# Kernel tuning notes

Measured on AMD Instinct MI355X. Metric: run time of the kernel, lower is better.

Reference implementation:

```python
import jax, jax.numpy as jnp
import numpy as np

IN_CH = 16
OUT_CH = 64
G = 4
K = 3
EXP_CH = G * IN_CH * OUT_CH  # 4096 expanded channels
SET_LEN = G * IN_CH          # 64 indices per pooling set
B, H, W = 8, 56, 56


def setup_inputs() -> dict:
    key = jax.random.key(0)
    k1, k2, k3, k4 = jax.random.split(key, 4)
    x = jax.random.normal(k1, (B, IN_CH, H, W), dtype=jnp.float32)
    # grouped conv weight: [out_channels=EXP_CH, in_ch/groups=1, K, K]
    weight = jax.random.normal(k2, (EXP_CH, 1, K, K), dtype=jnp.float32) * 0.1
    bias = jax.random.normal(k3, (EXP_CH,), dtype=jnp.float32) * 0.1
    # channel_idx_sets: OUT_CH sets, each SET_LEN indices into the EXP_CH channels
    idx_sets = jax.random.randint(k4, (OUT_CH, SET_LEN), 0, EXP_CH, dtype=jnp.int32)
    return {"x": x, "weight": weight, "bias": bias, "idx_sets": idx_sets}


def reference(x, weight, bias, idx_sets):
    # Grouped conv2d: groups = IN_CH, output channels = G*IN_CH*OUT_CH
    out = jax.lax.conv_general_dilated(
        x, weight,
        window_strides=(1, 1),
        padding=((1, 1), (1, 1)),
        feature_group_count=IN_CH,
        dimension_numbers=("NCHW", "OIHW", "NCHW"),
    )
    out = out + bias[None, :, None, None]  # [B, EXP_CH, H, W]
    # FusedMultiPool: for each output channel j, max over channels idx_sets[j]
    gathered = out[:, idx_sets]            # [B, OUT_CH, SET_LEN, H, W]
    return jnp.max(gathered, axis=2)       # [B, OUT_CH, H, W]
```

## Files before the change

### kernel.cpp

```cpp
#include <hip/hip_runtime.h>

#define IN_CH    16
#define OUT_CH   64
#define SET_LEN  64
#define BB       8
#define HH       56
#define WW       56

#define TILEROWS 8
#define NTILES   7
#define LDSROWS  (TILEROWS + 2)
#define LROW     56
#define LDS_XN   (IN_CH * LDSROWS * LROW)
#define NVEC     (IN_CH * LDSROWS * 14)

#define WS_NEEDED (OUT_CH * SET_LEN * 12 * 4)

typedef float f32x2 __attribute__((ext_vector_type(2)));
typedef float f32x4 __attribute__((ext_vector_type(4)));

static __device__ __forceinline__ f32x2 splat2(float s) { return (f32x2){s, s}; }

static __device__ __forceinline__ f32x2 pk_mul_slo(unsigned long long sp, f32x2 b) {
    f32x2 d;
    asm("v_pk_mul_f32 %0, %1, %2 op_sel:[0,0] op_sel_hi:[0,1]"
        : "=v"(d) : "s"(sp), "v"(b));
    return d;
}
static __device__ __forceinline__ f32x2 pk_mul_shi(unsigned long long sp, f32x2 b) {
    f32x2 d;
    asm("v_pk_mul_f32 %0, %1, %2 op_sel:[1,0] op_sel_hi:[1,1]"
        : "=v"(d) : "s"(sp), "v"(b));
    return d;
}
static __device__ __forceinline__ f32x2 pk_fma_slo(unsigned long long sp, f32x2 b, f32x2 c) {
    f32x2 d;
    asm("v_pk_fma_f32 %0, %1, %2, %3 op_sel:[0,0,0] op_sel_hi:[0,1,1]"
        : "=v"(d) : "s"(sp), "v"(b), "v"(c));
    return d;
}
static __device__ __forceinline__ f32x2 pk_fma_shi(unsigned long long sp, f32x2 b, f32x2 c) {
    f32x2 d;
    asm("v_pk_fma_f32 %0, %1, %2, %3 op_sel:[1,0,0] op_sel_hi:[1,1,1]"
        : "=v"(d) : "s"(sp), "v"(b), "v"(c));
    return d;
}
static __device__ __forceinline__ f32x2 pk_add_vv(f32x2 a, f32x2 b) {
    f32x2 d;
    asm("v_pk_add_f32 %0, %1, %2 op_sel:[0,0] op_sel_hi:[1,1]"
        : "=v"(d) : "v"(a), "v"(b));
    return d;
}
static __device__ __forceinline__ f32x2 pk_add_shi(unsigned long long sp, f32x2 b) {
    f32x2 d;
    asm("v_pk_add_f32 %0, %1, %2 op_sel:[1,0] op_sel_hi:[1,1]"
        : "=v"(d) : "s"(sp), "v"(b));
    return d;
}

__global__ __launch_bounds__(64)
void rptn_presort(const float* __restrict__ w, const float* __restrict__ bias,
                  const int* __restrict__ idx, float* __restrict__ ws_w) {
    const int oc = blockIdx.x;
    const int t  = threadIdx.x;
    __shared__ int cnt[IN_CH], pos[IN_CH], eord[SET_LEN];

    if (t < IN_CH) cnt[t] = 0;
    __syncthreads();
    const int e = idx[oc * SET_LEN + t];
    const int c = e >> 8;
    atomicAdd(&cnt[c], 1);
    __syncthreads();
    if (t == 0) {
        int run = 0;
        for (int i = 0; i < IN_CH; ++i) { pos[i] = run; run += cnt[i]; }
    }
    __syncthreads();
    const int p = atomicAdd(&pos[c], 1);
    eord[p] = e;
    __syncthreads();

    const int    es  = eord[t];
    float*       dst = ws_w + ((size_t)oc * SET_LEN + t) * 12;
    const float* src = w + es * 9;
    #pragma unroll
    for (int i = 0; i < 9; ++i) dst[i] = src[i];
    dst[9]  = bias[es];
    dst[10] = __int_as_float(es >> 8);
    dst[11] = 0.0f;
}

__global__ __launch_bounds__(256, 2)
void rptn_fused_kernel(const float* __restrict__ x,
                       const float* __restrict__ ws_w,
                       float*       __restrict__ out) {
    const int oc   = blockIdx.x;
    const int tile = blockIdx.y;
    const int b    = blockIdx.z;
    const int tid  = threadIdx.x;
    const int tx   = tid & 63;
    const int grp  = __builtin_amdgcn_readfirstlane(tid >> 6);

    __shared__ float s_x[LDS_XN];

    const int r0 = tile * TILEROWS;
    const float* xb = x + (size_t)b * IN_CH * HH * WW;
    #pragma unroll
    for (int it = 0; it < 9; ++it) {
        const int v = tid + it * 256;
        if (it < 8 || v < NVEC) {
            const int c   = v / (LDSROWS * 14);
            const int rem = v - c * (LDSROWS * 14);
            const int r   = rem / 14;
            const int q   = rem - r * 14;
            const int gr  = r0 - 1 + r;
            f32x4 val = {0, 0, 0, 0};
            if ((unsigned)gr < (unsigned)HH)
                val = *(const f32x4*)(xb + (c * HH + gr) * WW + q * 4);
            *(f32x4*)&s_x[(c * LDSROWS + r) * LROW + q * 4] = val;
        }
    }
    __syncthreads();

    const bool  lanev = (tx < WW);
    const int   txr   = lanev ? tx : 0;
    const int   txl   = (txr > 0)  ? txr - 1 : 0;
    const int   txp   = (txr < 55) ? txr + 1 : 55;
    const float lm    = (txr == 0)  ? 0.0f : 1.0f;
    const float rm    = (txr == 55) ? 0.0f : 1.0f;

    f32x2 acc = { -__builtin_inff(), -__builtin_inff() };
    int ccur = -1;
    f32x2 v00={0,0},v01={0,0},v02={0,0};
    f32x2 v10={0,0},v11={0,0},v12={0,0};
    f32x2 v20={0,0},v21={0,0},v22={0,0};

    const ulonglong2* wt = (const ulonglong2*)ws_w + (size_t)oc * SET_LEN * 3;

    #pragma unroll 4
    for (int k = 0; k < SET_LEN; ++k) {
        const ulonglong2 A = wt[k * 3 + 0];
        const ulonglong2 B = wt[k * 3 + 1];
        const ulonglong2 C = wt[k * 3 + 2];
        const int c = (int)(unsigned int)(C.y & 0xffffffffULL);
        if (c != ccur) {
            ccur = c;
            const float* sp = &s_x[(c * LDSROWS + grp * 2) * LROW];
            const float n00=sp[txl]*lm,        n01=sp[txr],        n02=sp[txp]*rm;
            const float n10=sp[LROW+txl]*lm,   n11=sp[LROW+txr],   n12=sp[LROW+txp]*rm;
            const float n20=sp[2*LROW+txl]*lm, n21=sp[2*LROW+txr], n22=sp[2*LROW+txp]*rm;
            const float n30=sp[3*LROW+txl]*lm, n31=sp[3*LROW+txr], n32=sp[3*LROW+txp]*rm;
            v00=(f32x2){n00,n10}; v01=(f32x2){n01,n11}; v02=(f32x2){n02,n12};
            v10=(f32x2){n10,n20}; v11=(f32x2){n11,n21}; v12=(f32x2){n12,n22};
            v20=(f32x2){n20,n30}; v21=(f32x2){n21,n31}; v22=(f32x2){n22,n32};
        }
        f32x2 t0 = pk_mul_slo(A.x, v00);
        t0       = pk_fma_shi(A.x, v01, t0);
        t0       = pk_fma_slo(A.y, v02, t0);
        f32x2 t1 = pk_mul_shi(A.y, v10);
        t1       = pk_fma_slo(B.x, v11, t1);
        t1       = pk_fma_shi(B.x, v12, t1);
        f32x2 t2 = pk_mul_slo(B.y, v20);
        t2       = pk_fma_shi(B.y, v21, t2);
        t2       = pk_fma_slo(C.x, v22, t2);
        f32x2 s  = pk_add_vv(t0, t1);
        s        = pk_add_vv(s, t2);
        s        = pk_add_shi(C.x, s);
        acc.x = fmaxf(acc.x, s.x);
        acc.y = fmaxf(acc.y, s.y);
    }

    if (lanev) {
        const size_t o = (((size_t)b * OUT_CH + oc) * HH + (r0 + grp * 2)) * WW + tx;
        out[o]      = acc.x;
        out[o + WW] = acc.y;
    }
}

__global__ __launch_bounds__(256, 2)
void rptn_fused_fallback(const float* __restrict__ x,
                         const float* __restrict__ w,
                         const float* __restrict__ bias,
                         const int*   __restrict__ idx,
                         float*       __restrict__ out) {
    const int oc   = blockIdx.x;
    const int tile = blockIdx.y;
    const int b    = blockIdx.z;
    const int tid  = threadIdx.x;
    const int tx   = tid & 63;
    const int grp  = __builtin_amdgcn_readfirstlane(tid >> 6);

    __shared__ float s_x[LDS_XN];
    __shared__ f32x4 s_w[SET_LEN * 3];
    __shared__ int   s_cnt[IN_CH];
    __shared__ int   s_pos[IN_CH];
    __shared__ int   s_eord[SET_LEN];

    if (tid < IN_CH) s_cnt[tid] = 0;
    __syncthreads();
    int my_e = 0;
    if (tid < SET_LEN) {
        my_e = idx[oc * SET_LEN + tid];
        atomicAdd(&s_cnt[my_e >> 8], 1);
    }
    __syncthreads();
    if (tid == 0) {
        int run = 0;
        for (int c = 0; c < IN_CH; ++c) { s_pos[c] = run; run += s_cnt[c]; }
    }
    __syncthreads();
    if (tid < SET_LEN) {
        int p = atomicAdd(&s_pos[my_e >> 8], 1);
        s_eord[p] = my_e;
    }
    __syncthreads();

    float* s_wf = (float*)s_w;
    for (int i = tid; i < SET_LEN * 12; i += 256) {
        const int j    = i / 12;
        const int comp = i - j * 12;
        const int e    = s_eord[j];
        float v;
        if (comp < 9)        v = w[e * 9 + comp];
        else if (comp == 9)  v = bias[e];
        else if (comp == 10) v = __int_as_float(e >> 8);
        else                 v = 0.0f;
        s_wf[j * 12 + comp] = v;
    }

    const int r0 = tile * TILEROWS;
    const float* xb = x + (size_t)b * IN_CH * HH * WW;
    #pragma unroll
    for (int it = 0; it < 9; ++it) {
        const int v = tid + it * 256;
        if (it < 8 || v < NVEC) {
            const int c   = v / (LDSROWS * 14);
            const int rem = v - c * (LDSROWS * 14);
            const int r   = rem / 14;
            const int q   = rem - r * 14;
            const int gr  = r0 - 1 + r;
            f32x4 val = {0, 0, 0, 0};
            if ((unsigned)gr < (unsigned)HH)
                val = *(const f32x4*)(xb + (c * HH + gr) * WW + q * 4);
            *(f32x4*)&s_x[(c * LDSROWS + r) * LROW + q * 4] = val;
        }
    }
    __syncthreads();

    const bool  lanev = (tx < WW);
    const int   txr   = lanev ? tx : 0;
    const int   txl   = (txr > 0)  ? txr - 1 : 0;
    const int   txp   = (txr < 55) ? txr + 1 : 55;
    const float lm    = (txr == 0)  ? 0.0f : 1.0f;
    const float rm    = (txr == 55) ? 0.0f : 1.0f;

    f32x2 acc = { -__builtin_inff(), -__builtin_inff() };
    int ccur = -1;
    f32x2 v00={0,0},v01={0,0},v02={0,0};
    f32x2 v10={0,0},v11={0,0},v12={0,0};
    f32x2 v20={0,0},v21={0,0},v22={0,0};

    #pragma unroll 2
    for (int k = 0; k < SET_LEN; ++k) {
        const f32x4 q0 = s_w[k * 3 + 0];
        const f32x4 q1 = s_w[k * 3 + 1];
        const f32x4 q2 = s_w[k * 3 + 2];
        const int c = __float_as_int(q2.z);
        if (c != ccur) {
            ccur = c;
            const float* sp = &s_x[(c * LDSROWS + grp * 2) * LROW];
            const float n00=sp[txl]*lm,        n01=sp[txr],        n02=sp[txp]*rm;
            const float n10=sp[LROW+txl]*lm,   n11=sp[LROW+txr],   n12=sp[LROW+txp]*rm;
            const float n20=sp[2*LROW+txl]*lm, n21=sp[2*LROW+txr], n22=sp[2*LROW+txp]*rm;
            const float n30=sp[3*LROW+txl]*lm, n31=sp[3*LROW+txr], n32=sp[3*LROW+txp]*rm;
            v00=(f32x2){n00,n10}; v01=(f32x2){n01,n11}; v02=(f32x2){n02,n12};
            v10=(f32x2){n10,n20}; v11=(f32x2){n11,n21}; v12=(f32x2){n12,n22};
            v20=(f32x2){n20,n30}; v21=(f32x2){n21,n31}; v22=(f32x2){n22,n32};
        }
        f32x2 t0 = __builtin_elementwise_fma(splat2(q0.z), v02,
                   __builtin_elementwise_fma(splat2(q0.y), v01,
                   __builtin_elementwise_fma(splat2(q0.x), v00, splat2(q2.y))));
        f32x2 t1 = __builtin_elementwise_fma(splat2(q1.y), v12,
                   __builtin_elementwise_fma(splat2(q1.x), v11,
                                             splat2(q0.w) * v10));
        f32x2 t2 = __builtin_elementwise_fma(splat2(q2.x), v22,
                   __builtin_elementwise_fma(splat2(q1.w), v21,
                                             splat2(q1.z) * v20));
        const f32x2 s = t0 + (t1 + t2);
        acc.x = fmaxf(acc.x, s.x);
        acc.y = fmaxf(acc.y, s.y);
    }

    if (lanev) {
        const size_t o = (((size_t)b * OUT_CH + oc) * HH + (r0 + grp * 2)) * WW + tx;
        out[o]      = acc.x;
        out[o + WW] = acc.y;
    }
}

extern "C" void kernel_launch(void* const* d_in, const int* in_sizes, int n_in,
                              void* d_out, int out_size, void* d_ws, size_t ws_size,
                              hipStream_t stream) {
    const float* x    = (const float*)d_in[0];
    const float* w    = (const float*)d_in[1];
    const float* bias = (const float*)d_in[2];
    const int*   idx  = (const int*)d_in[3];
    float*       out  = (float*)d_out;

    dim3 grid(OUT_CH, NTILES, BB);
    dim3 block(256);

    if (ws_size >= (size_t)WS_NEEDED) {
        float* ws_w = (float*)d_ws;
        rptn_presort<<<dim3(OUT_CH), dim3(64), 0, stream>>>(w, bias, idx, ws_w);
        rptn_fused_kernel<<<grid, block, 0, stream>>>(x, ws_w, out);
    } else {
        rptn_fused_fallback<<<grid, block, 0, stream>>>(x, w, bias, idx, out);
    }
}
```

Baseline: 116.8 us.

## Pack channel ids into scalar words and fully unroll pooling loop with vector weight loads

The presort kernel now also writes eight packed 32-bit words per output channel holding the 4-bit input-channel id of each sorted entry, so the main kernel can decide neighbourhood reloads from wave-uniform scalar bits. The 64-entry loop is fully unrolled, and the weights are read through a VGPR-offset base (a forced v_mov zero) so they arrive as vector loads fed to the packed math as VGPR operands. The goal is to remove per-iteration scalar load latency and loop overhead. In exchange it adds a larger code body, extra VGPR pressure, and per-lane redundant weight loads.

New measurement: 166.4 us. +42.5%, slower.

```diff
diff --git a/kernel.cpp b/kernel.cpp
--- a/kernel.cpp
+++ b/kernel.cpp
@@ -14,35 +14,37 @@
 #define LDS_XN   (IN_CH * LDSROWS * LROW)
 #define NVEC     (IN_CH * LDSROWS * 14)
 
-#define WS_NEEDED (OUT_CH * SET_LEN * 12 * 4)
+#define WS_CW_OFF 0
+#define WS_W_OFF  2048
+#define WS_NEEDED (WS_W_OFF + OUT_CH * SET_LEN * 12 * 4)
 
 typedef float f32x2 __attribute__((ext_vector_type(2)));
 typedef float f32x4 __attribute__((ext_vector_type(4)));
 
 static __device__ __forceinline__ f32x2 splat2(float s) { return (f32x2){s, s}; }
 
-static __device__ __forceinline__ f32x2 pk_mul_slo(unsigned long long sp, f32x2 b) {
+static __device__ __forceinline__ f32x2 pk_mul_vlo(unsigned long long wp, f32x2 b) {
     f32x2 d;
     asm("v_pk_mul_f32 %0, %1, %2 op_sel:[0,0] op_sel_hi:[0,1]"
-        : "=v"(d) : "s"(sp), "v"(b));
-    return d;
-}
-static __device__ __forceinline__ f32x2 pk_mul_shi(unsigned long long sp, f32x2 b) {
+        : "=v"(d) : "v"(wp), "v"(b));
+    return d;
+}
+static __device__ __forceinline__ f32x2 pk_mul_vhi(unsigned long long wp, f32x2 b) {
     f32x2 d;
     asm("v_pk_mul_f32 %0, %1, %2 op_sel:[1,0] op_sel_hi:[1,1]"
-        : "=v"(d) : "s"(sp), "v"(b));
-    return d;
-}
-static __device__ __forceinline__ f32x2 pk_fma_slo(unsigned long long sp, f32x2 b, f32x2 c) {
+        : "=v"(d) : "v"(wp), "v"(b));
+    return d;
+}
+static __device__ __forceinline__ f32x2 pk_fma_vlo(unsigned long long wp, f32x2 b, f32x2 c) {
     f32x2 d;
     asm("v_pk_fma_f32 %0, %1, %2, %3 op_sel:[0,0,0] op_sel_hi:[0,1,1]"
-        : "=v"(d) : "s"(sp), "v"(b), "v"(c));
-    return d;
-}
-static __device__ __forceinline__ f32x2 pk_fma_shi(unsigned long long sp, f32x2 b, f32x2 c) {
+        : "=v"(d) : "v"(wp), "v"(b), "v"(c));
+    return d;
+}
+static __device__ __forceinline__ f32x2 pk_fma_vhi(unsigned long long wp, f32x2 b, f32x2 c) {
     f32x2 d;
     asm("v_pk_fma_f32 %0, %1, %2, %3 op_sel:[1,0,0] op_sel_hi:[1,1,1]"
-        : "=v"(d) : "s"(sp), "v"(b), "v"(c));
+        : "=v"(d) : "v"(wp), "v"(b), "v"(c));
     return d;
 }
 static __device__ __forceinline__ f32x2 pk_add_vv(f32x2 a, f32x2 b) {
@@ -51,16 +53,17 @@
         : "=v"(d) : "v"(a), "v"(b));
     return d;
 }
-static __device__ __forceinline__ f32x2 pk_add_shi(unsigned long long sp, f32x2 b) {
+static __device__ __forceinline__ f32x2 pk_add_vhi(unsigned long long wp, f32x2 b) {
     f32x2 d;
     asm("v_pk_add_f32 %0, %1, %2 op_sel:[1,0] op_sel_hi:[1,1]"
-        : "=v"(d) : "s"(sp), "v"(b));
+        : "=v"(d) : "v"(wp), "v"(b));
     return d;
 }
 
 __global__ __launch_bounds__(64)
 void rptn_presort(const float* __restrict__ w, const float* __restrict__ bias,
-                  const int* __restrict__ idx, float* __restrict__ ws_w) {
+                  const int* __restrict__ idx, unsigned* __restrict__ ws_cw,
+                  float* __restrict__ ws_w) {
     const int oc = blockIdx.x;
     const int t  = threadIdx.x;
     __shared__ int cnt[IN_CH], pos[IN_CH], eord[SET_LEN];
@@ -88,10 +91,19 @@
     dst[9]  = bias[es];
     dst[10] = __int_as_float(es >> 8);
     dst[11] = 0.0f;
+
+    if (t < 8) {
+        unsigned wd = 0;
+        #pragma unroll
+        for (int j = 0; j < 8; ++j)
+            wd |= ((unsigned)(eord[t * 8 + j] >> 8)) << (4 * j);
+        ws_cw[oc * 8 + t] = wd;
+    }
 }
 
 __global__ __launch_bounds__(256, 2)
 void rptn_fused_kernel(const float* __restrict__ x,
+                       const unsigned* __restrict__ ws_cw,
                        const float* __restrict__ ws_w,
                        float*       __restrict__ out) {
     const int oc   = blockIdx.x;
@@ -120,6 +132,15 @@
             *(f32x4*)&s_x[(c * LDSROWS + r) * LROW + q * 4] = val;
         }
     }
+
+    const unsigned* cwp = ws_cw + oc * 8;
+    const unsigned cw0 = cwp[0], cw1 = cwp[1], cw2 = cwp[2], cw3 = cwp[3];
+    const unsigned cw4 = cwp[4], cw5 = cwp[5], cw6 = cwp[6], cw7 = cwp[7];
+
+    unsigned zoff;
+    asm volatile("v_mov_b32 %0, 0" : "=v"(zoff));
+    const char* wbase = (const char*)(ws_w + (size_t)oc * SET_LEN * 12) + zoff;
+
     __syncthreads();
 
     const bool  lanev = (tx < WW);
@@ -135,40 +156,51 @@
     f32x2 v10={0,0},v11={0,0},v12={0,0};
     f32x2 v20={0,0},v21={0,0},v22={0,0};
 
-    const ulonglong2* wt = (const ulonglong2*)ws_w + (size_t)oc * SET_LEN * 3;
-
-    #pragma unroll 4
-    for (int k = 0; k < SET_LEN; ++k) {
-        const ulonglong2 A = wt[k * 3 + 0];
-        const ulonglong2 B = wt[k * 3 + 1];
-        const ulonglong2 C = wt[k * 3 + 2];
-        const int c = (int)(unsigned int)(C.y & 0xffffffffULL);
-        if (c != ccur) {
-            ccur = c;
-            const float* sp = &s_x[(c * LDSROWS + grp * 2) * LROW];
-            const float n00=sp[txl]*lm,        n01=sp[txr],        n02=sp[txp]*rm;
-            const float n10=sp[LROW+txl]*lm,   n11=sp[LROW+txr],   n12=sp[LROW+txp]*rm;
-            const float n20=sp[2*LROW+txl]*lm, n21=sp[2*LROW+txr], n22=sp[2*LROW+txp]*rm;
-            const float n30=sp[3*LROW+txl]*lm, n31=sp[3*LROW+txr], n32=sp[3*LROW+txp]*rm;
-            v00=(f32x2){n00,n10}; v01=(f32x2){n01,n11}; v02=(f32x2){n02,n12};
-            v10=(f32x2){n10,n20}; v11=(f32x2){n11,n21}; v12=(f32x2){n12,n22};
-            v20=(f32x2){n20,n30}; v21=(f32x2){n21,n31}; v22=(f32x2){n22,n32};
-        }
-        f32x2 t0 = pk_mul_slo(A.x, v00);
-        t0       = pk_fma_shi(A.x, v01, t0);
-        t0       = pk_fma_slo(A.y, v02, t0);
-        f32x2 t1 = pk_mul_shi(A.y, v10);
-        t1       = pk_fma_slo(B.x, v11, t1);
-        t1       = pk_fma_shi(B.x, v12, t1);
-        f32x2 t2 = pk_mul_slo(B.y, v20);
-        t2       = pk_fma_shi(B.y, v21, t2);
-        t2       = pk_fma_slo(C.x, v22, t2);
-        f32x2 s  = pk_add_vv(t0, t1);
-        s        = pk_add_vv(s, t2);
-        s        = pk_add_shi(C.x, s);
-        acc.x = fmaxf(acc.x, s.x);
-        acc.y = fmaxf(acc.y, s.y);
-    }
+#define NBLOAD(C_) do {                                                        \
+        const float* sp = &s_x[((C_) * LDSROWS + grp * 2) * LROW];             \
+        const float n00=sp[txl]*lm,        n01=sp[txr],        n02=sp[txp]*rm; \
+        const float n10=sp[LROW+txl]*lm,   n11=sp[LROW+txr],   n12=sp[LROW+txp]*rm; \
+        const float n20=sp[2*LROW+txl]*lm, n21=sp[2*LROW+txr], n22=sp[2*LROW+txp]*rm; \
+        const float n30=sp[3*LROW+txl]*lm, n31=sp[3*LROW+txr], n32=sp[3*LROW+txp]*rm; \
+        v00=(f32x2){n00,n10}; v01=(f32x2){n01,n11}; v02=(f32x2){n02,n12};      \
+        v10=(f32x2){n10,n20}; v11=(f32x2){n11,n21}; v12=(f32x2){n12,n22};      \
+        v20=(f32x2){n20,n30}; v21=(f32x2){n21,n31}; v22=(f32x2){n22,n32};      \
+    } while (0)
+
+#define ENT(K, CW, J) do {                                                     \
+        const int c_ = (int)(((CW) >> (4 * (J))) & 15u);                       \
+        if (c_ != ccur) { ccur = c_; NBLOAD(c_); }                             \
+        const char* wp_ = wbase + (K) * 48;                                    \
+        const ulonglong2 A  = *(const ulonglong2*)(wp_);                       \
+        const ulonglong2 Bq = *(const ulonglong2*)(wp_ + 16);                  \
+        const ulonglong2 Cq = *(const ulonglong2*)(wp_ + 32);                  \
+        f32x2 t0 = pk_mul_vlo(A.x,  v00);                                      \
+        t0       = pk_fma_vhi(A.x,  v01, t0);                                  \
+        t0       = pk_fma_vlo(A.y,  v02, t0);                                  \
+        f32x2 t1 = pk_mul_vhi(A.y,  v10);                                      \
+        t1       = pk_fma_vlo(Bq.x, v11, t1);                                  \
+        t1       = pk_fma_vhi(Bq.x, v12, t1);                                  \
+        f32x2 t2 = pk_mul_vlo(Bq.y, v20);                                      \
+        t2       = pk_fma_vhi(Bq.y, v21, t2);                                  \
+        t2       = pk_fma_vlo(Cq.x, v22, t2);                                  \
+        f32x2 s_ = pk_add_vv(t0, t1);                                          \
+        s_       = pk_add_vv(s_, t2);                                          \
+        s_       = pk_add_vhi(Cq.x, s_);                                       \
+        acc.x = fmaxf(acc.x, s_.x);                                            \
+        acc.y = fmaxf(acc.y, s_.y);                                            \
+    } while (0)
+
+#define GRP8(G, CW)                                                            \
+    ENT((G)*8+0, CW, 0); ENT((G)*8+1, CW, 1); ENT((G)*8+2, CW, 2);             \
+    ENT((G)*8+3, CW, 3); ENT((G)*8+4, CW, 4); ENT((G)*8+5, CW, 5);             \
+    ENT((G)*8+6, CW, 6); ENT((G)*8+7, CW, 7);
+
+    GRP8(0, cw0) GRP8(1, cw1) GRP8(2, cw2) GRP8(3, cw3)
+    GRP8(4, cw4) GRP8(5, cw5) GRP8(6, cw6) GRP8(7, cw7)
+
+#undef GRP8
+#undef ENT
+#undef NBLOAD
 
     if (lanev) {
         const size_t o = (((size_t)b * OUT_CH + oc) * HH + (r0 + grp * 2)) * WW + tx;
@@ -311,9 +343,10 @@
     dim3 block(256);
 
     if (ws_size >= (size_t)WS_NEEDED) {
-        float* ws_w = (float*)d_ws;
-        rptn_presort<<<dim3(OUT_CH), dim3(64), 0, stream>>>(w, bias, idx, ws_w);
-        rptn_fused_kernel<<<grid, block, 0, stream>>>(x, ws_w, out);
+        unsigned* ws_cw = (unsigned*)((char*)d_ws + WS_CW_OFF);
+        float*    ws_w  = (float*)((char*)d_ws + WS_W_OFF);
+        rptn_presort<<<dim3(OUT_CH), dim3(64), 0, stream>>>(w, bias, idx, ws_cw, ws_w);
+        rptn_fused_kernel<<<grid, block, 0, stream>>>(x, ws_cw, ws_w, out);
     } else {
         rptn_fused_fallback<<<grid, block, 0, stream>>>(x, w, bias, idx, out);
     }
```
